# Optimization experiments

Measured on AMD Instinct MI355X. Metric: run time of the kernel, lower is better.

## Reference

```python
import jax, jax.numpy as jnp
import numpy as np
import math

SIGMA_MIN = 0.1
SIGMA_MAX = 10.0
C = 2.0
LOG_2PI = math.log(2.0 * math.pi)

V, T, D, N = 32000, 128, 64, 512


def _clamp_params(mu, log_sigma, mu_c, log_sigma_c):
    lo, hi = math.log(SIGMA_MIN), math.log(SIGMA_MAX)
    b = math.sqrt(C)
    return (jnp.clip(mu, -b, b), jnp.clip(log_sigma, lo, hi),
            jnp.clip(mu_c, -b, b), jnp.clip(log_sigma_c, lo, hi))


def el_energy(mu_v, mu_t, sigma_v, sigma_t, d):
    # mu_v/sigma_v: (V,D); mu_t/sigma_t: (T,D) -> broadcast (V,T,D), reduce D
    s = sigma_v[:, None, :] + sigma_t[None, :, :]            # (V,T,D)
    det_fac = jnp.sum(jnp.log(s), axis=2)                    # (V,T)
    diff_mu = jnp.sum((mu_v[:, None, :] - mu_t[None, :, :]) ** 2 / s, axis=2)
    return -0.5 * (det_fac + diff_mu + d * LOG_2PI)


def kl_energy(mu_v, mu_t, log_sigma_v, log_sigma_t, d):
    sigma_v = jnp.exp(log_sigma_v)[:, None, :]               # (V,1,D)
    sigma_t = jnp.exp(log_sigma_t)[None, :, :]               # (1,T,D)
    det_fac = jnp.sum(log_sigma_t, axis=1)[None, :] - jnp.sum(log_sigma_v, axis=1)[:, None]
    trace_fac = jnp.sum(sigma_v / sigma_t, axis=2)           # (V,T)
    diff_mu = jnp.sum((mu_v[:, None, :] - mu_t[None, :, :]) ** 2 / sigma_t, axis=2)
    return 0.5 * (det_fac - d + trace_fac + diff_mu)


def setup_inputs() -> dict:
    key = jax.random.key(0)
    ks = jax.random.split(key, 5)
    mu = 0.02 * jax.random.normal(ks[0], (V, D), dtype=jnp.float32)
    log_sigma = 0.02 * jax.random.normal(ks[1], (V, D), dtype=jnp.float32)
    mu_c = 0.02 * jax.random.normal(ks[2], (T, D), dtype=jnp.float32)
    log_sigma_c = 0.02 * jax.random.normal(ks[3], (T, D), dtype=jnp.float32)
    x = jax.random.normal(ks[4], (T, N), dtype=jnp.float32)
    return {"x": x, "mu": mu, "log_sigma": log_sigma,
            "mu_c": mu_c, "log_sigma_c": log_sigma_c, "t": 0}


def reference(x, mu, log_sigma, mu_c, log_sigma_c, t):
    d = mu.shape[1]
    mu, log_sigma, mu_c, log_sigma_c = _clamp_params(mu, log_sigma, mu_c, log_sigma_c)
    if t == 0:
        mu_v, ls_v = mu, log_sigma
    else:
        mu_v = jax.lax.stop_gradient(mu)
        ls_v = jax.lax.stop_gradient(log_sigma)
    energy = el_energy(mu_v, mu_c, jnp.exp(ls_v), jnp.exp(log_sigma_c), d)  # (V,T)
    w = jax.nn.softmax(energy, axis=0)                        # softmax over vocab dim
    kl_dis = kl_energy(mu, mu_c, log_sigma, log_sigma_c, d)   # (V,T)
    out = w @ x                                               # (V,N)
    return (out, kl_dis)
```

## Files before the change

kernel.cpp:

```cpp
#include <hip/hip_runtime.h>
#include <math.h>

#define V 32000
#define T 128
#define DD 64
#define NN 512

typedef float f32x4 __attribute__((ext_vector_type(4)));

constexpr float kB     = 1.4142135623730951f;
constexpr float kLSLO  = -2.302585092994046f;
constexpr float kLSHI  =  2.302585092994046f;
constexpr float kLN2   =  0.6931471805599453f;
constexpr float kDLOG2PI = 117.6241322501981f;

__device__ __forceinline__ float clampf(float x, float lo, float hi) {
    return fminf(fmaxf(x, lo), hi);
}

__global__ void k_prep(const float* __restrict__ mu_c, const float* __restrict__ ls_c,
                       float* __restrict__ st_td, float* __restrict__ mc_td,
                       float* __restrict__ rs_td, float* __restrict__ sumlsc) {
    int t = threadIdx.x;
    if (t >= T) return;
    float acc = 0.f;
    for (int d = 0; d < DD; ++d) {
        float lc = clampf(ls_c[t * DD + d], kLSLO, kLSHI);
        float st = __expf(lc);
        st_td[t * DD + d] = st;
        rs_td[t * DD + d] = 1.0f / st;
        mc_td[t * DD + d] = clampf(mu_c[t * DD + d], -kB, kB);
        acc += lc;
    }
    sumlsc[t] = acc;
}

__global__ void __launch_bounds__(256, 2)
k_energy_kl(const float* __restrict__ mu, const float* __restrict__ ls,
            const float* __restrict__ st_td, const float* __restrict__ mc_td,
            const float* __restrict__ rs_td, const float* __restrict__ sumlsc,
            float* __restrict__ eT, float* __restrict__ kl_out) {
    const int v  = blockIdx.y * 256 + threadIdx.x;
    const int t0 = blockIdx.x * 32;

    __shared__ float klt[32][257];

    float sv[DD], muv[DD];
    float slv = 0.f;
    const float* lrow = ls + (size_t)v * DD;
    const float* mrow = mu + (size_t)v * DD;
    #pragma unroll
    for (int q = 0; q < DD / 4; ++q) {
        const float4 l4 = *reinterpret_cast<const float4*>(lrow + q * 4);
        const float4 m4 = *reinterpret_cast<const float4*>(mrow + q * 4);
        const float lf[4] = {l4.x, l4.y, l4.z, l4.w};
        const float mf[4] = {m4.x, m4.y, m4.z, m4.w};
        #pragma unroll
        for (int r = 0; r < 4; ++r) {
            const float lsv = clampf(lf[r], kLSLO, kLSHI);
            slv += lsv;
            sv[q * 4 + r]  = __expf(lsv);
            muv[q * 4 + r] = clampf(mf[r], -kB, kB);
        }
    }

    #pragma unroll 1
    for (int tl = 0; tl < 32; ++tl) {
        const int t = t0 + tl;
        const float* st_r = st_td + t * DD;
        const float* mc_r = mc_td + t * DD;
        const float* rs_r = rs_td + t * DD;
        float det = 0.f, ae = 0.f, akl = 0.f;
        #pragma unroll
        for (int dc = 0; dc < 4; ++dc) {
            float prod = 1.f;
            #pragma unroll
            for (int dd = 0; dd < 16; ++dd) {
                const int d = dc * 16 + dd;
                const float st = st_r[d];
                const float mc = mc_r[d];
                const float rs = rs_r[d];
                const float s  = sv[d] + st;
                prod *= s;
                const float diff = muv[d] - mc;
                const float d2   = diff * diff;
                ae  = __builtin_fmaf(d2, __builtin_amdgcn_rcpf(s), ae);
                akl = __builtin_fmaf(sv[d] + d2, rs, akl);
            }
            det += __log2f(prod);
        }
        eT[(size_t)t * V + v] = -0.5f * (det * kLN2 + ae + kDLOG2PI);
        klt[tl][threadIdx.x] = 0.5f * (sumlsc[t] - slv - 64.0f + akl);
    }

    __syncthreads();
    const int tc = threadIdx.x & 31;
    const int vb = threadIdx.x >> 5;
    #pragma unroll 1
    for (int p = 0; p < 32; ++p) {
        const int vl = p * 8 + vb;
        kl_out[(size_t)(blockIdx.y * 256 + vl) * T + t0 + tc] = klt[tc][vl];
    }
}

__global__ void k_colred(const float* __restrict__ eT,
                         float* __restrict__ pmax, float* __restrict__ psum) {
    const int seg = blockIdx.x;
    const int t   = blockIdx.y;
    const float* row = eT + (size_t)t * V + seg * 8000;
    float m = -INFINITY, s = 0.f;
    for (int i = threadIdx.x; i < 8000; i += 256) {
        const float e  = row[i];
        const float nm = fmaxf(m, e);
        s = s * __expf(m - nm) + __expf(e - nm);
        m = nm;
    }
    __shared__ float sm[256], ss[256];
    sm[threadIdx.x] = m; ss[threadIdx.x] = s;
    __syncthreads();
    for (int w = 128; w > 0; w >>= 1) {
        if (threadIdx.x < w) {
            const float mA = sm[threadIdx.x], mB = sm[threadIdx.x + w];
            const float nm = fmaxf(mA, mB);
            ss[threadIdx.x] = ss[threadIdx.x] * __expf(mA - nm)
                            + ss[threadIdx.x + w] * __expf(mB - nm);
            sm[threadIdx.x] = nm;
        }
        __syncthreads();
    }
    if (threadIdx.x == 0) { pmax[t * 4 + seg] = sm[0]; psum[t * 4 + seg] = ss[0]; }
}

__global__ void k_finalize(const float* __restrict__ pmax, const float* __restrict__ psum,
                           float* __restrict__ mrow, float* __restrict__ rden) {
    const int t = threadIdx.x;
    if (t >= T) return;
    float m = -INFINITY, s = 0.f;
    for (int k = 0; k < 4; ++k) {
        const float mB = pmax[t * 4 + k], sB = psum[t * 4 + k];
        const float nm = fmaxf(m, mB);
        s = s * __expf(m - nm) + sB * __expf(mB - nm);
        m = nm;
    }
    mrow[t] = m;
    rden[t] = 1.0f / s;
}

__global__ void k_scale_x(const float* __restrict__ x, const float* __restrict__ rden,
                          float* __restrict__ xs) {
    const int i = blockIdx.x * 256 + threadIdx.x;
    const int t = i >> 9;
    xs[i] = x[i] * rden[t];
}

__global__ void __launch_bounds__(256) k_gemm(const float* __restrict__ eT,
                                              const float* __restrict__ mrow,
                                              const float* __restrict__ xs,
                                              float* __restrict__ out) {
    const int v0   = blockIdx.x * 64;
    const int pass = blockIdx.y;
    __shared__ float pl[128][64];
    for (int i = 0; i < 32; ++i) {
        const int idx = i * 256 + threadIdx.x;
        const int t = idx >> 6, vl = idx & 63;
        const float e = eT[(size_t)t * V + v0 + vl];
        pl[t][vl] = __expf(e - mrow[t]);
    }
    __syncthreads();

    const int va = (threadIdx.x & 15) * 4;
    const int ng = threadIdx.x >> 4;
    const int nb = pass * 128 + ng * 8;

    float acc[4][8];
    #pragma unroll
    for (int i = 0; i < 4; ++i)
        #pragma unroll
        for (int k = 0; k < 8; ++k) acc[i][k] = 0.f;

    #pragma unroll 2
    for (int t = 0; t < 128; ++t) {
        const float4 p4 = *reinterpret_cast<const float4*>(&pl[t][va]);
        const float4 xa = *reinterpret_cast<const float4*>(&xs[t * NN + nb]);
        const float4 xb = *reinterpret_cast<const float4*>(&xs[t * NN + nb + 4]);
        const float pv[4] = {p4.x, p4.y, p4.z, p4.w};
        const float xv[8] = {xa.x, xa.y, xa.z, xa.w, xb.x, xb.y, xb.z, xb.w};
        #pragma unroll
        for (int i = 0; i < 4; ++i)
            #pragma unroll
            for (int k = 0; k < 8; ++k)
                acc[i][k] = __builtin_fmaf(pv[i], xv[k], acc[i][k]);
    }
    #pragma unroll
    for (int i = 0; i < 4; ++i) {
        f32x4 lo = {acc[i][0], acc[i][1], acc[i][2], acc[i][3]};
        f32x4 hi = {acc[i][4], acc[i][5], acc[i][6], acc[i][7]};
        __builtin_nontemporal_store(lo,
            reinterpret_cast<f32x4*>(&out[(size_t)(v0 + va + i) * NN + nb]));
        __builtin_nontemporal_store(hi,
            reinterpret_cast<f32x4*>(&out[(size_t)(v0 + va + i) * NN + nb + 4]));
    }
}

extern "C" void kernel_launch(void* const* d_in, const int* in_sizes, int n_in,
                              void* d_out, int out_size, void* d_ws, size_t ws_size,
                              hipStream_t stream) {
    const float* x    = (const float*)d_in[0];
    const float* mu   = (const float*)d_in[1];
    const float* ls   = (const float*)d_in[2];
    const float* mu_c = (const float*)d_in[3];
    const float* ls_c = (const float*)d_in[4];

    float* out = (float*)d_out;
    float* kl  = out + (size_t)V * NN;

    float* ws      = (float*)d_ws;
    float* eT      = ws;
    float* st_td   = eT + (size_t)T * V;
    float* mc_td   = st_td + T * DD;
    float* rs_td   = mc_td + T * DD;
    float* sumlsc  = rs_td + T * DD;
    float* pmax    = sumlsc + T;
    float* psum    = pmax + T * 4;
    float* mrow    = psum + T * 4;
    float* rden    = mrow + T;
    float* xs      = rden + T;

    k_prep<<<1, 128, 0, stream>>>(mu_c, ls_c, st_td, mc_td, rs_td, sumlsc);
    k_energy_kl<<<dim3(4, V / 256), 256, 0, stream>>>(mu, ls, st_td, mc_td, rs_td, sumlsc, eT, kl);
    k_colred<<<dim3(4, T), 256, 0, stream>>>(eT, pmax, psum);
    k_finalize<<<1, 128, 0, stream>>>(pmax, psum, mrow, rden);
    k_scale_x<<<(T * NN) / 256, 256, 0, stream>>>(x, rden, xs);
    k_gemm<<<dim3(V / 64, 4), 256, 0, stream>>>(eT, mrow, xs, out);
}
```

Baseline: 283.1 us.

## Raise occupancy in energy and GEMM kernels, parallelize prep across blocks

The energy/KL kernel now handles 16 t-columns per block instead of 32, doubling the grid, and its launch bound is raised to 4 blocks per CU, which constrains register use. The GEMM now stages exp-probabilities through a half-size shared tile in two 64-row phases and software-prefetches x rows into registers two steps ahead. k_prep is spread across 128 blocks with a wave shuffle reduction instead of running serially in one block. The intent is more occupancy and better latency hiding; the tighter register budget may spill the 128-float per-thread arrays, and recomputing the v-row preload for twice as many blocks adds redundant work.

```diff
diff --git a/kernel.cpp b/kernel.cpp
--- a/kernel.cpp
+++ b/kernel.cpp
@@ -5,6 +5,7 @@
 #define T 128
 #define DD 64
 #define NN 512
+#define TCH 16
 
 typedef float f32x4 __attribute__((ext_vector_type(4)));
 
@@ -21,29 +22,27 @@
 __global__ void k_prep(const float* __restrict__ mu_c, const float* __restrict__ ls_c,
                        float* __restrict__ st_td, float* __restrict__ mc_td,
                        float* __restrict__ rs_td, float* __restrict__ sumlsc) {
-    int t = threadIdx.x;
-    if (t >= T) return;
-    float acc = 0.f;
-    for (int d = 0; d < DD; ++d) {
-        float lc = clampf(ls_c[t * DD + d], kLSLO, kLSHI);
-        float st = __expf(lc);
-        st_td[t * DD + d] = st;
-        rs_td[t * DD + d] = 1.0f / st;
-        mc_td[t * DD + d] = clampf(mu_c[t * DD + d], -kB, kB);
-        acc += lc;
-    }
-    sumlsc[t] = acc;
-}
-
-__global__ void __launch_bounds__(256, 2)
+    const int t = blockIdx.x;
+    const int d = threadIdx.x;
+    float lc = clampf(ls_c[t * DD + d], kLSLO, kLSHI);
+    const float st = __expf(lc);
+    st_td[t * DD + d] = st;
+    rs_td[t * DD + d] = 1.0f / st;
+    mc_td[t * DD + d] = clampf(mu_c[t * DD + d], -kB, kB);
+    float s = lc;
+    for (int o = 32; o > 0; o >>= 1) s += __shfl_down(s, o);
+    if (d == 0) sumlsc[t] = s;
+}
+
+__global__ void __launch_bounds__(256, 4)
 k_energy_kl(const float* __restrict__ mu, const float* __restrict__ ls,
             const float* __restrict__ st_td, const float* __restrict__ mc_td,
             const float* __restrict__ rs_td, const float* __restrict__ sumlsc,
             float* __restrict__ eT, float* __restrict__ kl_out) {
     const int v  = blockIdx.y * 256 + threadIdx.x;
-    const int t0 = blockIdx.x * 32;
-
-    __shared__ float klt[32][257];
+    const int t0 = blockIdx.x * TCH;
+
+    __shared__ float klt[TCH][257];
 
     float sv[DD], muv[DD];
     float slv = 0.f;
@@ -65,7 +64,7 @@
     }
 
     #pragma unroll 1
-    for (int tl = 0; tl < 32; ++tl) {
+    for (int tl = 0; tl < TCH; ++tl) {
         const int t = t0 + tl;
         const float* st_r = st_td + t * DD;
         const float* mc_r = mc_td + t * DD;
@@ -94,11 +93,11 @@
     }
 
     __syncthreads();
-    const int tc = threadIdx.x & 31;
-    const int vb = threadIdx.x >> 5;
+    const int tc = threadIdx.x & (TCH - 1);
+    const int vb = threadIdx.x / TCH;
     #pragma unroll 1
-    for (int p = 0; p < 32; ++p) {
-        const int vl = p * 8 + vb;
+    for (int p = 0; p < 16; ++p) {
+        const int vl = p * 16 + vb;
         kl_out[(size_t)(blockIdx.y * 256 + vl) * T + t0 + tc] = klt[tc][vl];
     }
 }
@@ -157,20 +156,13 @@
                                               const float* __restrict__ mrow,
                                               const float* __restrict__ xs,
                                               float* __restrict__ out) {
-    const int v0   = blockIdx.x * 64;
-    const int pass = blockIdx.y;
-    __shared__ float pl[128][64];
-    for (int i = 0; i < 32; ++i) {
-        const int idx = i * 256 + threadIdx.x;
-        const int t = idx >> 6, vl = idx & 63;
-        const float e = eT[(size_t)t * V + v0 + vl];
-        pl[t][vl] = __expf(e - mrow[t]);
-    }
-    __syncthreads();
+    const int v0 = blockIdx.x * 64;
+    const int nbase = blockIdx.y * 128;
+    __shared__ float pl[64][64];
 
     const int va = (threadIdx.x & 15) * 4;
     const int ng = threadIdx.x >> 4;
-    const int nb = pass * 128 + ng * 8;
+    const int nb = nbase + ng * 8;
 
     float acc[4][8];
     #pragma unroll
@@ -178,19 +170,44 @@
         #pragma unroll
         for (int k = 0; k < 8; ++k) acc[i][k] = 0.f;
 
-    #pragma unroll 2
-    for (int t = 0; t < 128; ++t) {
-        const float4 p4 = *reinterpret_cast<const float4*>(&pl[t][va]);
-        const float4 xa = *reinterpret_cast<const float4*>(&xs[t * NN + nb]);
-        const float4 xb = *reinterpret_cast<const float4*>(&xs[t * NN + nb + 4]);
-        const float pv[4] = {p4.x, p4.y, p4.z, p4.w};
-        const float xv[8] = {xa.x, xa.y, xa.z, xa.w, xb.x, xb.y, xb.z, xb.w};
-        #pragma unroll
-        for (int i = 0; i < 4; ++i)
+    #pragma unroll 1
+    for (int h = 0; h < 2; ++h) {
+        if (h) __syncthreads();
+        #pragma unroll
+        for (int i = 0; i < 16; ++i) {
+            const int idx = i * 256 + threadIdx.x;
+            const int t = idx >> 6, vl = idx & 63;
+            const float e = eT[(size_t)(h * 64 + t) * V + v0 + vl];
+            pl[t][vl] = __expf(e - mrow[h * 64 + t]);
+        }
+        __syncthreads();
+
+        const float* xh = xs + (h * 64) * NN + nb;
+        float4 xA[2], xB[2];
+        xA[0] = *reinterpret_cast<const float4*>(xh);
+        xB[0] = *reinterpret_cast<const float4*>(xh + 4);
+        xA[1] = *reinterpret_cast<const float4*>(xh + NN);
+        xB[1] = *reinterpret_cast<const float4*>(xh + NN + 4);
+
+        #pragma unroll 2
+        for (int tt = 0; tt < 64; ++tt) {
+            const float4 p4 = *reinterpret_cast<const float4*>(&pl[tt][va]);
+            const float4 xa = xA[tt & 1];
+            const float4 xb = xB[tt & 1];
+            if (tt < 62) {
+                xA[tt & 1] = *reinterpret_cast<const float4*>(xh + (tt + 2) * NN);
+                xB[tt & 1] = *reinterpret_cast<const float4*>(xh + (tt + 2) * NN + 4);
+            }
+            const float pv[4] = {p4.x, p4.y, p4.z, p4.w};
+            const float xv[8] = {xa.x, xa.y, xa.z, xa.w, xb.x, xb.y, xb.z, xb.w};
             #pragma unroll
-            for (int k = 0; k < 8; ++k)
-                acc[i][k] = __builtin_fmaf(pv[i], xv[k], acc[i][k]);
-    }
+            for (int i = 0; i < 4; ++i)
+                #pragma unroll
+                for (int k = 0; k < 8; ++k)
+                    acc[i][k] = __builtin_fmaf(pv[i], xv[k], acc[i][k]);
+        }
+    }
+
     #pragma unroll
     for (int i = 0; i < 4; ++i) {
         f32x4 lo = {acc[i][0], acc[i][1], acc[i][2], acc[i][3]};
@@ -226,8 +243,8 @@
     float* rden    = mrow + T;
     float* xs      = rden + T;
 
-    k_prep<<<1, 128, 0, stream>>>(mu_c, ls_c, st_td, mc_td, rs_td, sumlsc);
-    k_energy_kl<<<dim3(4, V / 256), 256, 0, stream>>>(mu, ls, st_td, mc_td, rs_td, sumlsc, eT, kl);
+    k_prep<<<T, 64, 0, stream>>>(mu_c, ls_c, st_td, mc_td, rs_td, sumlsc);
+    k_energy_kl<<<dim3(T / TCH, V / 256), 256, 0, stream>>>(mu, ls, st_td, mc_td, rs_td, sumlsc, eT, kl);
     k_colred<<<dim3(4, T), 256, 0, stream>>>(eT, pmax, psum);
     k_finalize<<<1, 128, 0, stream>>>(pmax, psum, mrow, rden);
     k_scale_x<<<(T * NN) / 256, 256, 0, stream>>>(x, rden, xs);
```

After: 345.7 us. 22.1% more time.
